# Kernel tuning notes

Hardware: AMD Instinct MI355X
Metric: run time of the kernel (lower is better)

Reference implementation:

```python
import jax, jax.numpy as jnp
import numpy as np

DIM = 1024

def setup_inputs() -> dict:
    key = jax.random.key(0)
    ks = jax.random.split(key, 6)
    B, T, D = 8, 2048, DIM
    s = 1.0 / np.sqrt(D)
    x = jax.random.normal(ks[0], (B, T, D), dtype=jnp.float32)
    Wq = jax.random.normal(ks[1], (D, D), dtype=jnp.float32) * s
    Wk = jax.random.normal(ks[2], (D, D), dtype=jnp.float32) * s
    Wv = jax.random.normal(ks[3], (D, D), dtype=jnp.float32) * s
    Wp = jax.random.normal(ks[4], (D, D), dtype=jnp.float32) * s
    bp = jax.random.normal(ks[5], (D,), dtype=jnp.float32) * 0.01
    return {"x": x, "Wq": Wq, "Wk": Wk, "Wv": Wv, "Wp": Wp, "bp": bp}

def reference(x, Wq, Wk, Wv, Wp, bp):
    # x: [b, t, d]; weights stored as [d_in, d_out] (torch Linear applies x @ W.T;
    # here we bake the transpose into the stored matrix).
    scale = x.shape[-1] ** (-0.5)
    q = jnp.einsum('btd,de->bte', x, Wq)
    k = jnp.einsum('btd,de->bte', x, Wk)
    v = jnp.einsum('btd,de->bte', x, Wv)
    attn = jax.nn.softmax(jnp.einsum('btd,bTd->btT', q, k) * scale, axis=-1)
    out = jnp.einsum('btT,bTd->btd', attn, v)
    return jnp.einsum('btd,de->bte', out, Wp) + bp
```

## Files before the change

kernel.cpp:

```cpp
#include <hip/hip_runtime.h>


typedef _Float16 half_t;
typedef _Float16 half8 __attribute__((ext_vector_type(8)));
typedef float floatx4 __attribute__((ext_vector_type(4)));

#define GLD16(gp, lp)                                                          \
    __builtin_amdgcn_global_load_lds(                                          \
        (const __attribute__((address_space(1))) void*)(gp),                   \
        (__attribute__((address_space(3))) void*)(lp), 16, 0, 0)

#define WAIT_VM0()  asm volatile("s_waitcnt vmcnt(0)" ::: "memory")
#define BARRIER()   do { asm volatile("" ::: "memory");                        \
                         __builtin_amdgcn_s_barrier();                         \
                         asm volatile("" ::: "memory"); } while (0)

template<int EPI>
__global__ __launch_bounds__(512, 2)
void gemm16(const half_t* __restrict__ A, const half_t* __restrict__ B,
            void* __restrict__ Cv, void* __restrict__ C2, void* __restrict__ C3,
            const float* __restrict__ bias, int K, int lda, int ldb, int ldc,
            long long bsA, long long bsB, long long bsC)
{
    __shared__ half_t As[2 * 2 * 128 * 64];
    __shared__ half_t Bs[2 * 2 * 128 * 64];

    const int tid  = threadIdx.x;
    const int lane = tid & 63;
    const int w    = tid >> 6;
    const int wm   = w >> 2;
    const int wn   = w & 3;

    int bx = blockIdx.x, by = blockIdx.y, bz = blockIdx.z;
    {
        const int gx = gridDim.x, gy = gridDim.y;
        const int nwg = gx * gy * (int)gridDim.z;
        int lid = (bz * gy + by) * gx + bx;
        const int qq = nwg >> 3, rr = nwg & 7;
        const int xcd = lid & 7, off = lid >> 3;
        lid = (xcd < rr ? xcd * (qq + 1) : rr * (qq + 1) + (xcd - rr) * qq) + off;
        bx = lid % gx; lid /= gx;
        by = lid % gy; bz = lid / gy;
    }
    const long long z = bz;
    const int rowBase = by * 256;
    const int colBase = bx * 256;

    const int srow = lane >> 3;
    const int schk = (lane & 7) ^ srow;
    const half_t* gp[4];
    int jstep[4];
    half_t* lp[4];
    #pragma unroll
    for (int i = 0; i < 4; ++i) {
        const bool ia = (i < 2);
        const int ld  = ia ? lda : ldb;
        const int rb  = (ia ? rowBase : colBase) + (i & 1) * 128 + w * 16 + srow;
        gp[i] = (ia ? A + z * bsA : B + z * bsB) + (long long)rb * ld + schk * 8;
        jstep[i] = 8 * ld;
        lp[i] = (ia ? As : Bs) + (i & 1) * 8192 + w * 1024;
    }

    const int fr  = lane & 15;
    const int q   = lane >> 4;
    const int rsw = fr & 7;
    const half_t* Abase = As + wm * 8192 + fr * 64;
    const half_t* Bbase = Bs + (wn >> 1) * 8192 + ((wn & 1) * 64 + fr) * 64;
    const int ko0 = ((0 + q) ^ rsw) * 8;
    const int ko1 = ((4 + q) ^ rsw) * 8;

    floatx4 acc[8][4];
    #pragma unroll
    for (int m = 0; m < 8; ++m)
        #pragma unroll
        for (int n = 0; n < 4; ++n)
            #pragma unroll
            for (int j = 0; j < 4; ++j) acc[m][n][j] = 0.0f;

    const int nIter = K >> 6;

    #pragma unroll
    for (int i = 0; i < 4; ++i) {
        GLD16(gp[i],            lp[i]);
        GLD16(gp[i] + jstep[i], lp[i] + 512);
    }
    WAIT_VM0();
    BARRIER();

    for (int t = 0; t < nIter; ++t) {
        const int cbuf = (t & 1) << 14;
        const int nbuf = 16384 - cbuf;
        half8 bf[4][2], afA[2][2], afB[2][2];

        #pragma unroll
        for (int n = 0; n < 4; ++n) {
            bf[n][0] = *(const half8*)(Bbase + cbuf + n * 1024 + ko0);
            bf[n][1] = *(const half8*)(Bbase + cbuf + n * 1024 + ko1);
        }
        afA[0][0] = *(const half8*)(Abase + cbuf + 0 * 1024 + ko0);
        afA[0][1] = *(const half8*)(Abase + cbuf + 0 * 1024 + ko1);
        afA[1][0] = *(const half8*)(Abase + cbuf + 1 * 1024 + ko0);
        afA[1][1] = *(const half8*)(Abase + cbuf + 1 * 1024 + ko1);

        if (t + 1 < nIter) {
            const int kk = (t + 1) << 6;
            #pragma unroll
            for (int i = 0; i < 4; ++i) {
                GLD16(gp[i] + kk,            lp[i] + nbuf);
                GLD16(gp[i] + kk + jstep[i], lp[i] + nbuf + 512);
            }
        }

        afB[0][0] = *(const half8*)(Abase + cbuf + 2 * 1024 + ko0);
        afB[0][1] = *(const half8*)(Abase + cbuf + 2 * 1024 + ko1);
        afB[1][0] = *(const half8*)(Abase + cbuf + 3 * 1024 + ko0);
        afB[1][1] = *(const half8*)(Abase + cbuf + 3 * 1024 + ko1);

        __builtin_amdgcn_s_setprio(1);
        #pragma unroll
        for (int ml = 0; ml < 2; ++ml)
            #pragma unroll
            for (int n = 0; n < 4; ++n)
                #pragma unroll
                for (int ks = 0; ks < 2; ++ks)
                    acc[ml][n] = __builtin_amdgcn_mfma_f32_16x16x32_f16(
                        afA[ml][ks], bf[n][ks], acc[ml][n], 0, 0, 0);
        __builtin_amdgcn_s_setprio(0);

        afA[0][0] = *(const half8*)(Abase + cbuf + 4 * 1024 + ko0);
        afA[0][1] = *(const half8*)(Abase + cbuf + 4 * 1024 + ko1);
        afA[1][0] = *(const half8*)(Abase + cbuf + 5 * 1024 + ko0);
        afA[1][1] = *(const half8*)(Abase + cbuf + 5 * 1024 + ko1);
        __builtin_amdgcn_s_setprio(1);
        #pragma unroll
        for (int ml = 0; ml < 2; ++ml)
            #pragma unroll
            for (int n = 0; n < 4; ++n)
                #pragma unroll
                for (int ks = 0; ks < 2; ++ks)
                    acc[2 + ml][n] = __builtin_amdgcn_mfma_f32_16x16x32_f16(
                        afB[ml][ks], bf[n][ks], acc[2 + ml][n], 0, 0, 0);
        __builtin_amdgcn_s_setprio(0);

        afB[0][0] = *(const half8*)(Abase + cbuf + 6 * 1024 + ko0);
        afB[0][1] = *(const half8*)(Abase + cbuf + 6 * 1024 + ko1);
        afB[1][0] = *(const half8*)(Abase + cbuf + 7 * 1024 + ko0);
        afB[1][1] = *(const half8*)(Abase + cbuf + 7 * 1024 + ko1);
        __builtin_amdgcn_s_setprio(1);
        #pragma unroll
        for (int ml = 0; ml < 2; ++ml)
            #pragma unroll
            for (int n = 0; n < 4; ++n)
                #pragma unroll
                for (int ks = 0; ks < 2; ++ks)
                    acc[4 + ml][n] = __builtin_amdgcn_mfma_f32_16x16x32_f16(
                        afA[ml][ks], bf[n][ks], acc[4 + ml][n], 0, 0, 0);
        __builtin_amdgcn_s_setprio(0);

        __builtin_amdgcn_s_setprio(1);
        #pragma unroll
        for (int ml = 0; ml < 2; ++ml)
            #pragma unroll
            for (int n = 0; n < 4; ++n)
                #pragma unroll
                for (int ks = 0; ks < 2; ++ks)
                    acc[6 + ml][n] = __builtin_amdgcn_mfma_f32_16x16x32_f16(
                        afB[ml][ks], bf[n][ks], acc[6 + ml][n], 0, 0, 0);
        __builtin_amdgcn_s_setprio(0);

        WAIT_VM0();
        BARRIER();
    }

    const int ecol = lane & 15;
    const int q4   = (lane >> 4) * 4;
    #pragma unroll
    for (int m = 0; m < 8; ++m) {
        #pragma unroll
        for (int n = 0; n < 4; ++n) {
            const int gcol = colBase + wn * 64 + n * 16 + ecol;
            #pragma unroll
            for (int r = 0; r < 4; ++r) {
                const int grow = rowBase + wm * 128 + m * 16 + q4 + r;
                float v = acc[m][n][r];
                if (EPI == 0) {
                    ((half_t*)Cv)[z * bsC + (long long)grow * ldc + gcol] = (half_t)v;
                } else if (EPI == 1) {
                    ((float*)Cv)[(long long)grow * ldc + gcol] = v + bias[gcol];
                } else {
                    const int mat = colBase >> 10;
                    const int c   = gcol & 1023;
                    if (mat == 0) {
                        ((half_t*)Cv)[(long long)grow * 1024 + c] = (half_t)(v * 0.03125f);
                    } else if (mat == 1) {
                        ((half_t*)C2)[(long long)grow * 1024 + c] = (half_t)v;
                    } else {
                        const long long bb = grow >> 11;
                        const long long tt = grow & 2047;
                        ((half_t*)C3)[bb * (1024LL * 2048) + (long long)c * 2048 + tt] = (half_t)v;
                    }
                }
            }
        }
    }
}

__global__ __launch_bounds__(256)
void cast16(const float* __restrict__ x, half_t* __restrict__ y)
{
    const long long i = ((long long)blockIdx.x * 256 + threadIdx.x) * 8;
    floatx4 a = *(const floatx4*)(x + i);
    floatx4 b = *(const floatx4*)(x + i + 4);
    half8 h;
    #pragma unroll
    for (int j = 0; j < 4; ++j) { h[j] = (half_t)a[j]; h[j + 4] = (half_t)b[j]; }
    *(half8*)(y + i) = h;
}

__global__ __launch_bounds__(256)
void cast_transpose4(const float* __restrict__ W0, const float* __restrict__ W1,
                     const float* __restrict__ W2, const float* __restrict__ W3,
                     half_t* __restrict__ WT)
{
    const float* W = (blockIdx.z == 0) ? W0 : (blockIdx.z == 1) ? W1
                   : (blockIdx.z == 2) ? W2 : W3;
    half_t* O = WT + (long long)blockIdx.z * 1024 * 1024;
    __shared__ float t[32][33];
    const int bx = blockIdx.x * 32, by = blockIdx.y * 32;
    const int tx = threadIdx.x, ty = threadIdx.y;
    #pragma unroll
    for (int i = 0; i < 32; i += 8)
        t[ty + i][tx] = W[(long long)(by + ty + i) * 1024 + bx + tx];
    __syncthreads();
    #pragma unroll
    for (int i = 0; i < 32; i += 8)
        O[(long long)(bx + ty + i) * 1024 + by + tx] = (half_t)t[tx][ty + i];
}

__global__ __launch_bounds__(256)
void softmax_rows(half_t* __restrict__ S)
{
    const long long base = (long long)blockIdx.x * 2048;
    const int t = threadIdx.x;
    half8 h = *(const half8*)(S + base + t * 8);
    float v[8];
    #pragma unroll
    for (int i = 0; i < 8; ++i) v[i] = (float)h[i];
    float m = -3.0e38f;
    #pragma unroll
    for (int i = 0; i < 8; ++i) m = fmaxf(m, v[i]);
    #pragma unroll
    for (int off = 32; off > 0; off >>= 1) m = fmaxf(m, __shfl_down(m, off));
    __shared__ float redm[4], reds[4];
    const int lane = t & 63, wid = t >> 6;
    if (lane == 0) redm[wid] = m;
    __syncthreads();
    const float M = fmaxf(fmaxf(redm[0], redm[1]), fmaxf(redm[2], redm[3]));
    float s = 0.f;
    #pragma unroll
    for (int i = 0; i < 8; ++i) { v[i] = __expf(v[i] - M); s += v[i]; }
    #pragma unroll
    for (int off = 32; off > 0; off >>= 1) s += __shfl_down(s, off);
    if (lane == 0) reds[wid] = s;
    __syncthreads();
    const float inv = 1.0f / (reds[0] + reds[1] + reds[2] + reds[3]);
    #pragma unroll
    for (int i = 0; i < 8; ++i) h[i] = (half_t)(v[i] * inv);
    *(half8*)(S + base + t * 8) = h;
}

extern "C" void kernel_launch(void* const* d_in, const int* in_sizes, int n_in,
                              void* d_out, int out_size, void* d_ws, size_t ws_size,
                              hipStream_t stream)
{
    const float* x  = (const float*)d_in[0];
    const float* Wq = (const float*)d_in[1];
    const float* Wk = (const float*)d_in[2];
    const float* Wv = (const float*)d_in[3];
    const float* Wp = (const float*)d_in[4];
    const float* bp = (const float*)d_in[5];
    float* out = (float*)d_out;

    char* ws = (char*)d_ws;
    const long long MB = 1024LL * 1024LL;
    half_t* WqkvT = (half_t*)(ws + 0 * MB);
    half_t* WpT   = (half_t*)(ws + 6 * MB);
    half_t* q     = (half_t*)(ws + 8 * MB);
    half_t* k     = (half_t*)(ws + 40 * MB);
    half_t* vT    = (half_t*)(ws + 72 * MB);
    half_t* x16   = (half_t*)(ws + 104 * MB);
    half_t* S     = (half_t*)(ws + 104 * MB);

    dim3 blk(512);
    cast16<<<8192, dim3(256), 0, stream>>>(x, x16);
    cast_transpose4<<<dim3(32, 32, 4), dim3(32, 8), 0, stream>>>(Wq, Wk, Wv, Wp, WqkvT);

    gemm16<2><<<dim3(12, 64, 1), blk, 0, stream>>>(
        x16, WqkvT, q, k, vT, nullptr, 1024, 1024, 1024, 0, 0, 0, 0);

    gemm16<0><<<dim3(8, 8, 8), blk, 0, stream>>>(
        q, k, S, nullptr, nullptr, nullptr, 1024, 1024, 1024, 2048,
        2048LL * 1024, 2048LL * 1024, 2048LL * 2048);

    softmax_rows<<<8 * 2048, dim3(256), 0, stream>>>(S);

    gemm16<0><<<dim3(4, 8, 8), blk, 0, stream>>>(
        S, vT, q, nullptr, nullptr, nullptr, 2048, 2048, 2048, 1024,
        2048LL * 2048, 1024LL * 2048, 2048LL * 1024);

    gemm16<1><<<dim3(4, 64, 1), blk, 0, stream>>>(
        q, WpT, out, nullptr, nullptr, bp, 1024, 1024, 1024, 1024, 0, 0, 0);
}
```

Measured before the change: 490.4 us.

## Add smaller-tile 128x128 GEMM kernel for QKV projection

Adds a new GEMM kernel with 128x128 tiles, 256 threads, K-step 32 and a double-buffered LDS pipeline, and uses it for the fused QKV projection. The other GEMMs keep the 256x256 kernel. The 3-way epilogue now picks its output matrix per column rather than per block. The smaller tile gives more workgroups and better CU coverage on the QKV GEMM. In exchange it loses data reuse and uses a shorter K step per barrier.

New measurement: 501.5 us. +2.3%, slower.

```diff
diff --git a/kernel.cpp b/kernel.cpp
--- a/kernel.cpp
+++ b/kernel.cpp
@@ -16,20 +16,44 @@
                          asm volatile("" ::: "memory"); } while (0)
 
 template<int EPI>
-__global__ __launch_bounds__(512, 2)
-void gemm16(const half_t* __restrict__ A, const half_t* __restrict__ B,
-            void* __restrict__ Cv, void* __restrict__ C2, void* __restrict__ C3,
-            const float* __restrict__ bias, int K, int lda, int ldb, int ldc,
-            long long bsA, long long bsB, long long bsC)
-{
-    __shared__ half_t As[2 * 2 * 128 * 64];
-    __shared__ half_t Bs[2 * 2 * 128 * 64];
+__device__ __forceinline__ void store_elem(
+    void* Cv, void* C2, void* C3, const float* bias,
+    long long z, long long bsC, int ldc, int grow, int gcol, float v)
+{
+    if (EPI == 0) {
+        ((half_t*)Cv)[z * bsC + (long long)grow * ldc + gcol] = (half_t)v;
+    } else if (EPI == 1) {
+        ((float*)Cv)[(long long)grow * ldc + gcol] = v + bias[gcol];
+    } else {
+        const int mat = gcol >> 10;
+        const int c   = gcol & 1023;
+        if (mat == 0) {
+            ((half_t*)Cv)[(long long)grow * 1024 + c] = (half_t)(v * 0.03125f);
+        } else if (mat == 1) {
+            ((half_t*)C2)[(long long)grow * 1024 + c] = (half_t)v;
+        } else {
+            const long long bb = grow >> 11;
+            const long long tt = grow & 2047;
+            ((half_t*)C3)[bb * (1024LL * 2048) + (long long)c * 2048 + tt] = (half_t)v;
+        }
+    }
+}
+
+template<int EPI>
+__global__ __launch_bounds__(256, 4)
+void gemmA(const half_t* __restrict__ A, const half_t* __restrict__ B,
+           void* __restrict__ Cv, void* __restrict__ C2, void* __restrict__ C3,
+           const float* __restrict__ bias, int K, int lda, int ldb, int ldc,
+           long long bsA, long long bsB, long long bsC)
+{
+    __shared__ half_t As[2 * 128 * 32];
+    __shared__ half_t Bs[2 * 128 * 32];
 
     const int tid  = threadIdx.x;
     const int lane = tid & 63;
     const int w    = tid >> 6;
-    const int wm   = w >> 2;
-    const int wn   = w & 3;
+    const int wm   = w >> 1;
+    const int wn   = w & 1;
 
     int bx = blockIdx.x, by = blockIdx.y, bz = blockIdx.z;
     {
@@ -43,6 +67,117 @@
         by = lid % gy; bz = lid / gy;
     }
     const long long z = bz;
+    const int rowBase = by * 128;
+    const int colBase = bx * 128;
+
+    const int lrow = lane >> 2;
+    const int scol = (((lane & 3) ^ ((lane >> 3) & 3))) * 8;
+
+    const half_t* gptr[4];
+    int  lofs[4];
+    bool isA[4];
+    #pragma unroll
+    for (int j = 0; j < 4; ++j) {
+        const int g = w * 4 + j;
+        if (g < 8) {
+            gptr[j] = A + z * bsA + (long long)(rowBase + g * 16 + lrow) * lda + scol;
+            lofs[j] = g * 16 * 32;
+            isA[j]  = true;
+        } else {
+            gptr[j] = B + z * bsB + (long long)(colBase + (g - 8) * 16 + lrow) * ldb + scol;
+            lofs[j] = (g - 8) * 16 * 32;
+            isA[j]  = false;
+        }
+    }
+
+    floatx4 acc[4][4];
+    #pragma unroll
+    for (int m = 0; m < 4; ++m)
+        #pragma unroll
+        for (int n = 0; n < 4; ++n)
+            #pragma unroll
+            for (int j = 0; j < 4; ++j) acc[m][n][j] = 0.0f;
+
+    const int fr  = lane & 15;
+    const int fks = (((lane >> 4) ^ ((lane >> 1) & 3))) * 8;
+    const int nIter = K >> 5;
+
+    #pragma unroll
+    for (int j = 0; j < 4; ++j)
+        GLD16(gptr[j], isA[j] ? &As[lofs[j]] : &Bs[lofs[j]]);
+    WAIT_VM0();
+    BARRIER();
+
+    for (int it = 0; it < nIter; ++it) {
+        const int cur = (it & 1) * 4096;
+        const int nxt = 4096 - cur;
+        if (it + 1 < nIter) {
+            const int kk = (it + 1) << 5;
+            #pragma unroll
+            for (int j = 0; j < 4; ++j)
+                GLD16(gptr[j] + kk, isA[j] ? &As[nxt + lofs[j]] : &Bs[nxt + lofs[j]]);
+        }
+
+        half8 af[4], bf[4];
+        #pragma unroll
+        for (int m = 0; m < 4; ++m)
+            af[m] = *(const half8*)&As[cur + (wm * 64 + m * 16 + fr) * 32 + fks];
+        #pragma unroll
+        for (int n = 0; n < 4; ++n)
+            bf[n] = *(const half8*)&Bs[cur + (wn * 64 + n * 16 + fr) * 32 + fks];
+        #pragma unroll
+        for (int m = 0; m < 4; ++m)
+            #pragma unroll
+            for (int n = 0; n < 4; ++n)
+                acc[m][n] = __builtin_amdgcn_mfma_f32_16x16x32_f16(af[m], bf[n], acc[m][n], 0, 0, 0);
+
+        WAIT_VM0();
+        BARRIER();
+    }
+
+    const int ecol = lane & 15;
+    const int q4   = (lane >> 4) * 4;
+    #pragma unroll
+    for (int m = 0; m < 4; ++m)
+        #pragma unroll
+        for (int n = 0; n < 4; ++n) {
+            const int gcol = colBase + wn * 64 + n * 16 + ecol;
+            #pragma unroll
+            for (int r = 0; r < 4; ++r)
+                store_elem<EPI>(Cv, C2, C3, bias, z, bsC, ldc,
+                                rowBase + wm * 64 + m * 16 + q4 + r, gcol,
+                                acc[m][n][r]);
+        }
+}
+
+template<int EPI>
+__global__ __launch_bounds__(512, 2)
+void gemmB(const half_t* __restrict__ A, const half_t* __restrict__ B,
+           void* __restrict__ Cv, void* __restrict__ C2, void* __restrict__ C3,
+           const float* __restrict__ bias, int K, int lda, int ldb, int ldc,
+           long long bsA, long long bsB, long long bsC)
+{
+    __shared__ half_t As[2 * 2 * 128 * 64];
+    __shared__ half_t Bs[2 * 2 * 128 * 64];
+
+    const int tid  = threadIdx.x;
+    const int lane = tid & 63;
+    const int w    = tid >> 6;
+    const int wm   = w >> 2;
+    const int wn   = w & 3;
+
+    int bx = blockIdx.x, by = blockIdx.y, bz = blockIdx.z;
+    {
+        const int gx = gridDim.x, gy = gridDim.y;
+        const int nwg = gx * gy * (int)gridDim.z;
+        int lid = (bz * gy + by) * gx + bx;
+        const int qq = nwg >> 3, rr = nwg & 7;
+        const int xcd = lid & 7, off = lid >> 3;
+        lid = (xcd < rr ? xcd * (qq + 1) : rr * (qq + 1) + (xcd - rr) * qq) + off;
+        bx = lid % gx; lid /= gx;
+        by = lid % gy; bz = lid / gy;
+    }
+    const long long z = bz;
     const int rowBase = by * 256;
     const int colBase = bx * 256;
 
@@ -175,34 +310,16 @@
     const int ecol = lane & 15;
     const int q4   = (lane >> 4) * 4;
     #pragma unroll
-    for (int m = 0; m < 8; ++m) {
+    for (int m = 0; m < 8; ++m)
         #pragma unroll
         for (int n = 0; n < 4; ++n) {
             const int gcol = colBase + wn * 64 + n * 16 + ecol;
             #pragma unroll
-            for (int r = 0; r < 4; ++r) {
-                const int grow = rowBase + wm * 128 + m * 16 + q4 + r;
-                float v = acc[m][n][r];
-                if (EPI == 0) {
-                    ((half_t*)Cv)[z * bsC + (long long)grow * ldc + gcol] = (half_t)v;
-                } else if (EPI == 1) {
-                    ((float*)Cv)[(long long)grow * ldc + gcol] = v + bias[gcol];
-                } else {
-                    const int mat = colBase >> 10;
-                    const int c   = gcol & 1023;
-                    if (mat == 0) {
-                        ((half_t*)Cv)[(long long)grow * 1024 + c] = (half_t)(v * 0.03125f);
-                    } else if (mat == 1) {
-                        ((half_t*)C2)[(long long)grow * 1024 + c] = (half_t)v;
-                    } else {
-                        const long long bb = grow >> 11;
-                        const long long tt = grow & 2047;
-                        ((half_t*)C3)[bb * (1024LL * 2048) + (long long)c * 2048 + tt] = (half_t)v;
-                    }
-                }
-            }
-        }
-    }
+            for (int r = 0; r < 4; ++r)
+                store_elem<EPI>(Cv, C2, C3, bias, z, bsC, ldc,
+                                rowBase + wm * 128 + m * 16 + q4 + r, gcol,
+                                acc[m][n][r]);
+        }
 }
 
 __global__ __launch_bounds__(256)
@@ -291,23 +408,22 @@
     half_t* x16   = (half_t*)(ws + 104 * MB);
     half_t* S     = (half_t*)(ws + 104 * MB);
 
-    dim3 blk(512);
     cast16<<<8192, dim3(256), 0, stream>>>(x, x16);
     cast_transpose4<<<dim3(32, 32, 4), dim3(32, 8), 0, stream>>>(Wq, Wk, Wv, Wp, WqkvT);
 
-    gemm16<2><<<dim3(12, 64, 1), blk, 0, stream>>>(
+    gemmA<2><<<dim3(24, 128, 1), dim3(256), 0, stream>>>(
         x16, WqkvT, q, k, vT, nullptr, 1024, 1024, 1024, 0, 0, 0, 0);
 
-    gemm16<0><<<dim3(8, 8, 8), blk, 0, stream>>>(
+    gemmB<0><<<dim3(8, 8, 8), dim3(512), 0, stream>>>(
         q, k, S, nullptr, nullptr, nullptr, 1024, 1024, 1024, 2048,
         2048LL * 1024, 2048LL * 1024, 2048LL * 2048);
 
     softmax_rows<<<8 * 2048, dim3(256), 0, stream>>>(S);
 
-    gemm16<0><<<dim3(4, 8, 8), blk, 0, stream>>>(
+    gemmB<0><<<dim3(4, 8, 8), dim3(512), 0, stream>>>(
         S, vT, q, nullptr, nullptr, nullptr, 2048, 2048, 2048, 1024,
         2048LL * 2048, 1024LL * 2048, 2048LL * 1024);
 
-    gemm16<1><<<dim3(4, 64, 1), blk, 0, stream>>>(
+    gemmB<1><<<dim3(4, 64, 1), dim3(512), 0, stream>>>(
         q, WpT, out, nullptr, nullptr, bp, 1024, 1024, 1024, 1024, 0, 0, 0);
 }
```
